# Performance work log

Hardware: AMD Instinct MI355X
Metric: run time of the kernel (lower is better)

Reference implementation:

```python
import jax, jax.numpy as jnp
import numpy as np

N = 100000   # nodes
E = 600000   # edges
K = 3        # TAGConv hops
EPS = 1e-5   # BatchNorm eps
SLOPE = 0.01 # LeakyReLU negative slope


def setup_inputs() -> dict:
    key = jax.random.key(0)
    ks = jax.random.split(key, 8)
    y = jax.random.normal(ks[0], (N, 128), dtype=jnp.float32)
    edge_index = jax.random.randint(ks[1], (2, E), 0, N, dtype=jnp.int64)
    edge_attr = jax.random.uniform(ks[2], (E,), dtype=jnp.float32)
    # TAGConv layer l has (K+1) weight matrices [in, out]; bias only on first two layers
    W1 = 0.1 * jax.random.normal(ks[3], (K + 1, 128, 128), dtype=jnp.float32)
    b1 = jnp.full((128,), 0.1, dtype=jnp.float32)
    W2 = 0.1 * jax.random.normal(ks[4], (K + 1, 128, 128), dtype=jnp.float32)
    b2 = jnp.full((128,), 0.1, dtype=jnp.float32)
    W3 = 0.1 * jax.random.normal(ks[5], (K + 1, 128, 64), dtype=jnp.float32)
    g1 = jnp.ones((128,), jnp.float32); be1 = jnp.zeros((128,), jnp.float32)
    g2 = jnp.ones((128,), jnp.float32); be2 = jnp.zeros((128,), jnp.float32)
    g3 = jnp.ones((64,), jnp.float32);  be3 = jnp.zeros((64,), jnp.float32)
    return dict(y=y, edge_index=edge_index, edge_attr=edge_attr,
                W1=W1, b1=b1, g1=g1, be1=be1,
                W2=W2, b2=b2, g2=g2, be2=be2,
                W3=W3, g3=g3, be3=be3)


def _tag_conv(x, W, b, src, dst, norm):
    # out = sum_{k=0..K} A_hat^k x @ W_k (+ b)
    out = x @ W[0]
    h = x
    for k in range(1, W.shape[0]):
        h = jax.ops.segment_sum(norm[:, None] * h[src], dst, num_segments=N)
        out = out + h @ W[k]
    return out if b is None else out + b


def _bn(x, g, b):
    # BatchNorm1d training mode: biased batch stats over nodes
    m = x.mean(axis=0)
    v = jnp.mean((x - m) ** 2, axis=0)
    return (x - m) * jax.lax.rsqrt(v + EPS) * g + b


def reference(y, edge_index, edge_attr, W1, b1, g1, be1, W2, b2, g2, be2, W3, g3, be3):
    src, dst = edge_index[0], edge_index[1]
    # gcn_norm (symmetric, no self-loops): D^{-1/2} A D^{-1/2}
    deg = jax.ops.segment_sum(edge_attr, dst, num_segments=N)
    dis = jnp.where(deg > 0, jax.lax.rsqrt(jnp.maximum(deg, 1e-12)), 0.0)
    norm = dis[src] * edge_attr * dis[dst]
    lrelu = lambda t: jax.nn.leaky_relu(t, SLOPE)
    x = lrelu(_bn(_tag_conv(y, W1, b1, src, dst, norm), g1, be1))
    x = lrelu(_bn(_tag_conv(x, W2, b2, src, dst, norm), g2, be2))
    x = lrelu(_bn(_tag_conv(x, W3, None, src, dst, norm), g3, be3))
    return x
```

## Files before the change

### kernel.cpp

```cpp
#include <hip/hip_runtime.h>
#include <hip/hip_bf16.h>

typedef unsigned short b16;
typedef __attribute__((ext_vector_type(8))) unsigned short us8;
typedef __attribute__((ext_vector_type(8))) short short8;
typedef __attribute__((ext_vector_type(4))) float float4v;

#define NN 100000
#define NE 600000

__device__ __forceinline__ float bf2f(b16 u) {
    return __uint_as_float(((unsigned)u) << 16);
}
__device__ __forceinline__ b16 f2bf(float f) {
    unsigned x = __float_as_uint(f);
    return (b16)((x + 0x7fffu + ((x >> 16) & 1u)) >> 16);
}

__global__ void k_detect(const void* __restrict__ y, const void* __restrict__ ei,
                         int* __restrict__ flags) {
    if (threadIdx.x == 0 && blockIdx.x == 0) {
        const b16* p = (const b16*)y;
        int f32 = 0;
        for (int i = 0; i < 128; ++i) {
            float v = bf2f(p[i]);
            if (!(fabsf(v) < 1e4f)) { f32 = 1; break; }
        }
        flags[0] = f32;
        const long long* q = (const long long*)ei;
        int i64 = 1;
        for (int i = 0; i < 4; ++i) {
            long long v = q[i];
            if (v < 0 || v >= NN) i64 = 0;
        }
        flags[1] = i64;
    }
}

__global__ void k_cvt(const void* __restrict__ in, float* __restrict__ out, int n,
                      const int* __restrict__ flags) {
    int i = blockIdx.x * blockDim.x + threadIdx.x;
    if (i >= n) return;
    out[i] = flags[0] ? ((const float*)in)[i] : bf2f(((const b16*)in)[i]);
}

__global__ void k_idx(const void* __restrict__ ei, int* __restrict__ src32,
                      int* __restrict__ dst32, const int* __restrict__ flags) {
    int e = blockIdx.x * blockDim.x + threadIdx.x;
    if (e >= NE) return;
    int s, d;
    if (flags[1]) {
        const long long* p = (const long long*)ei;
        s = (int)p[e];
        d = (int)p[NE + e];
    } else {
        const int* p = (const int*)ei;
        s = p[e];
        d = p[NE + e];
    }
    src32[e] = ((unsigned)s < NN) ? s : 0;
    dst32[e] = ((unsigned)d < NN) ? d : 0;
}

__global__ void k_degcnt(const int* __restrict__ dst, const void* __restrict__ ea,
                         float* __restrict__ deg, int* __restrict__ cnt,
                         const int* __restrict__ flags) {
    int e = blockIdx.x * blockDim.x + threadIdx.x;
    if (e >= NE) return;
    float w = flags[0] ? ((const float*)ea)[e] : bf2f(((const b16*)ea)[e]);
    int d = dst[e];
    unsafeAtomicAdd(&deg[d], w);
    atomicAdd(&cnt[d], 1);
}

__global__ void k_dis(float* deg) {
    int n = blockIdx.x * blockDim.x + threadIdx.x;
    if (n < NN) {
        float d = deg[n];
        deg[n] = (d > 0.f) ? rsqrtf(fmaxf(d, 1e-12f)) : 0.f;
    }
}

#define SCAN_B 1024
#define SCAN_NB ((NN + SCAN_B - 1) / SCAN_B)

__global__ __launch_bounds__(SCAN_B) void k_scan1(const int* __restrict__ cnt,
                                                  int* __restrict__ inc,
                                                  int* __restrict__ bsum) {
    __shared__ int s[SCAN_B];
    int i = blockIdx.x * SCAN_B + threadIdx.x;
    s[threadIdx.x] = (i < NN) ? cnt[i] : 0;
    __syncthreads();
    for (int off = 1; off < SCAN_B; off <<= 1) {
        int t = (threadIdx.x >= off) ? s[threadIdx.x - off] : 0;
        __syncthreads();
        s[threadIdx.x] += t;
        __syncthreads();
    }
    if (i < NN) inc[i] = s[threadIdx.x];
    if (threadIdx.x == SCAN_B - 1) bsum[blockIdx.x] = s[SCAN_B - 1];
}

__global__ void k_scan2(int* bsum) {
    if (threadIdx.x == 0 && blockIdx.x == 0) {
        int a = 0;
        for (int i = 0; i < SCAN_NB; ++i) {
            int t = bsum[i];
            bsum[i] = a;
            a += t;
        }
    }
}

__global__ void k_scan3(const int* __restrict__ inc, const int* __restrict__ bsum,
                        int* __restrict__ rowptr) {
    int i = blockIdx.x * blockDim.x + threadIdx.x;
    if (i == 0) rowptr[0] = 0;
    if (i < NN) rowptr[i + 1] = inc[i] + bsum[i / SCAN_B];
}

__global__ void k_fill(const int* __restrict__ src, const int* __restrict__ dst,
                       const void* __restrict__ ea, const float* __restrict__ dis,
                       const int* __restrict__ rowptr, int* __restrict__ fill,
                       int* __restrict__ csrc, float* __restrict__ cw,
                       const int* __restrict__ flags) {
    int e = blockIdx.x * blockDim.x + threadIdx.x;
    if (e >= NE) return;
    float a = flags[0] ? ((const float*)ea)[e] : bf2f(((const b16*)ea)[e]);
    int d = dst[e];
    int s = src[e];
    int pos = rowptr[d] + atomicAdd(&fill[d], 1);
    csrc[pos] = s;
    cw[pos] = dis[s] * a * dis[d];
}

__global__ void k_pack(const void* __restrict__ W, b16* __restrict__ Wp, int NC,
                       const int* __restrict__ flags) {
    int f = blockIdx.x * blockDim.x + threadIdx.x;
    int total = 512 * NC / 8;
    if (f >= total) return;
    int lane = f & 63;
    int rest = f >> 6;
    int CT = NC >> 4;
    int ct = rest % CT, ks = rest / CT;
    int k0 = 32 * ks + (lane >> 4) * 8;
    int col = 16 * ct + (lane & 15);
    us8 v;
#pragma unroll
    for (int j = 0; j < 8; ++j) {
        float x = flags[0] ? ((const float*)W)[(size_t)(k0 + j) * NC + col]
                           : bf2f(((const b16*)W)[(size_t)(k0 + j) * NC + col]);
        v[j] = f2bf(x);
    }
    *(us8*)&Wp[(size_t)f * 8] = v;
}

__global__ void k_cast(const void* __restrict__ y, b16* __restrict__ XC,
                       const int* __restrict__ flags) {
    int i = blockIdx.x * blockDim.x + threadIdx.x;
    if (i >= NN * 32) return;
    int row = i >> 5, cg = i & 31;
    float4 v;
    if (flags[0]) {
        v = ((const float4*)y)[i];
    } else {
        ushort4 u = ((const ushort4*)y)[i];
        v = make_float4(bf2f(u.x), bf2f(u.y), bf2f(u.z), bf2f(u.w));
    }
    ushort4 o;
    o.x = f2bf(v.x); o.y = f2bf(v.y); o.z = f2bf(v.z); o.w = f2bf(v.w);
    *(ushort4*)&XC[(size_t)row * 512 + 4 * cg] = o;
}

__global__ __launch_bounds__(256) void k_spmm(b16* __restrict__ XC, int ci, int co,
                                              const int* __restrict__ rowptr,
                                              const int* __restrict__ csrc,
                                              const float* __restrict__ cw) {
    int gid = blockIdx.x * blockDim.x + threadIdx.x;
    int node = gid >> 6;
    if (node >= NN) return;
    int lane = gid & 63;
    int grp = lane >> 4;
    int l15 = lane & 15;
    int beg = rowptr[node], end = rowptr[node + 1];

    float a0[8], a1[8];
#pragma unroll
    for (int j = 0; j < 8; ++j) {
        a0[j] = 0.f;
        a1[j] = 0.f;
    }
    int i = beg;
    for (; i + 7 < end; i += 8) {
        int e0 = i + grp, e1 = i + 4 + grp;
        int s0 = csrc[e0];
        float w0 = cw[e0];
        int s1 = csrc[e1];
        float w1 = cw[e1];
        us8 u0 = *(const us8*)&XC[(size_t)s0 * 512 + ci + 8 * l15];
        us8 u1 = *(const us8*)&XC[(size_t)s1 * 512 + ci + 8 * l15];
#pragma unroll
        for (int j = 0; j < 8; ++j) {
            a0[j] = fmaf(w0, bf2f(u0[j]), a0[j]);
            a1[j] = fmaf(w1, bf2f(u1[j]), a1[j]);
        }
    }
    for (; i < end; i += 4) {
        int e = i + grp;
        bool act = e < end;
        int ee = act ? e : (end - 1);
        float w = act ? cw[ee] : 0.f;
        int s = csrc[ee];
        us8 u = *(const us8*)&XC[(size_t)s * 512 + ci + 8 * l15];
#pragma unroll
        for (int j = 0; j < 8; ++j) a0[j] = fmaf(w, bf2f(u[j]), a0[j]);
    }
#pragma unroll
    for (int j = 0; j < 8; ++j) a0[j] += a1[j];
#pragma unroll
    for (int j = 0; j < 8; ++j) a0[j] += __shfl_xor(a0[j], 16);
#pragma unroll
    for (int j = 0; j < 8; ++j) a0[j] += __shfl_xor(a0[j], 32);
    if (grp == 0) {
        us8 o;
#pragma unroll
        for (int j = 0; j < 8; ++j) o[j] = f2bf(a0[j]);
        *(us8*)&XC[(size_t)node * 512 + co + 8 * l15] = o;
    }
}

template <int NC>
__global__ __launch_bounds__(256) void k_mgemm(const b16* __restrict__ XC,
                                               const b16* __restrict__ Wp,
                                               const float* __restrict__ bias,
                                               b16* __restrict__ OUT,
                                               float* __restrict__ gsum,
                                               float* __restrict__ gsq) {
    constexpr int CT = NC / 16;
    __shared__ b16 As[2][64 * 40];
    __shared__ b16 Bs[2][CT * 512];
    __shared__ float csum[NC], csq[NC];
    const int tid = threadIdx.x;
    const int wave = tid >> 6;
    const int lane = tid & 63;
    const int row0 = blockIdx.x * 64;
    const int quad = lane >> 4;
    const int l15 = lane & 15;

    float4v acc[CT];
#pragma unroll
    for (int ct = 0; ct < CT; ++ct) acc[ct] = (float4v)(0.f);
    for (int i = tid; i < NC; i += 256) {
        csum[i] = 0.f;
        csq[i] = 0.f;
    }

    const int arow = tid >> 2;
    const int apart = tid & 3;
    int grow = row0 + arow;
    if (grow >= NN) grow = NN - 1;
    const b16* gA = XC + (size_t)grow * 512 + apart * 8;
    b16* lA0 = &As[0][arow * 40 + apart * 8];
    b16* lA1 = &As[1][arow * 40 + apart * 8];

    *(us8*)lA0 = *(const us8*)gA;
    {
        const us8* gB = (const us8*)Wp;
#pragma unroll
        for (int q = 0; q < CT * 64 / 256; ++q)
            ((us8*)Bs[0])[q * 256 + tid] = gB[q * 256 + tid];
    }

    for (int ks = 0; ks < 16; ++ks) {
        int buf = ks & 1;
        __syncthreads();
        if (ks < 15) {
            *(us8*)(buf ? lA0 : lA1) = *(const us8*)(gA + 32 * (ks + 1));
            const us8* gB = (const us8*)(Wp + (size_t)(ks + 1) * CT * 512);
#pragma unroll
            for (int q = 0; q < CT * 64 / 256; ++q)
                ((us8*)Bs[buf ^ 1])[q * 256 + tid] = gB[q * 256 + tid];
        }
        short8 af = *(const short8*)&As[buf][(wave * 16 + l15) * 40 + quad * 8];
#pragma unroll
        for (int ct = 0; ct < CT; ++ct) {
            short8 bf = *(const short8*)&Bs[buf][ct * 512 + lane * 8];
            acc[ct] = __builtin_amdgcn_mfma_f32_16x16x32_bf16(af, bf, acc[ct], 0, 0, 0);
        }
    }

#pragma unroll
    for (int ct = 0; ct < CT; ++ct) {
        int col = 16 * ct + l15;
        float bv = bias ? bias[col] : 0.f;
        float s = 0.f, sq = 0.f;
#pragma unroll
        for (int r = 0; r < 4; ++r) {
            int row = row0 + wave * 16 + quad * 4 + r;
            if (row < NN) {
                float v = acc[ct][r] + bv;
                OUT[(size_t)row * NC + col] = f2bf(v);
                s += v;
                sq += v * v;
            }
        }
        s += __shfl_xor(s, 16);
        s += __shfl_xor(s, 32);
        sq += __shfl_xor(sq, 16);
        sq += __shfl_xor(sq, 32);
        if (quad == 0) {
            atomicAdd(&csum[col], s);
            atomicAdd(&csq[col], sq);
        }
    }
    __syncthreads();
    for (int i = tid; i < NC; i += 256) {
        unsafeAtomicAdd(&gsum[i], csum[i]);
        unsafeAtomicAdd(&gsq[i], csq[i]);
    }
}

__global__ void k_bnparam(const float* gsum, const float* gsq, const float* g,
                          const float* be, float* scale, float* shift, int ncols) {
    int c = threadIdx.x;
    if (c < ncols) {
        float m = gsum[c] * (1.f / NN);
        float v = gsq[c] * (1.f / NN) - m * m;
        v = fmaxf(v, 0.f);
        float s = rsqrtf(v + 1e-5f) * g[c];
        scale[c] = s;
        shift[c] = be[c] - m * s;
    }
}

__global__ void k_bnapply_mid(const b16* __restrict__ OUT,
                              const float* __restrict__ scale,
                              const float* __restrict__ shift, b16* __restrict__ XC) {
    int i = blockIdx.x * blockDim.x + threadIdx.x;
    if (i >= NN * 64) return;
    int row = i >> 6, c = (i & 63) * 2;
    ushort2 u = *(const ushort2*)&OUT[(size_t)row * 128 + c];
    float a = fmaf(bf2f(u.x), scale[c], shift[c]);
    float b = fmaf(bf2f(u.y), scale[c + 1], shift[c + 1]);
    a = a > 0.f ? a : 0.01f * a;
    b = b > 0.f ? b : 0.01f * b;
    ushort2 o;
    o.x = f2bf(a);
    o.y = f2bf(b);
    *(ushort2*)&XC[(size_t)row * 512 + c] = o;
}

__global__ void k_bnapply_last(const b16* __restrict__ OUT,
                               const float* __restrict__ scale,
                               const float* __restrict__ shift, void* __restrict__ dout,
                               const int* __restrict__ flags) {
    int i = blockIdx.x * blockDim.x + threadIdx.x;
    if (i >= NN * 64) return;
    int c = i & 63;
    float v = fmaf(bf2f(OUT[i]), scale[c], shift[c]);
    v = v > 0.f ? v : 0.01f * v;
    if (flags[0])
        ((float*)dout)[i] = v;
    else
        ((b16*)dout)[i] = f2bf(v);
}

#define PB_B1 0
#define PB_B2 128
#define PB_G1 256
#define PB_BE1 384
#define PB_G2 512
#define PB_BE2 640
#define PB_G3 768
#define PB_BE3 832
#define PB_SZ 896

extern "C" void kernel_launch(void* const* d_in, const int* in_sizes, int n_in,
                              void* d_out, int out_size, void* d_ws, size_t ws_size,
                              hipStream_t stream) {
    const void* y   = d_in[0];
    const void* ei  = d_in[1];
    const void* ea  = d_in[2];
    const void* W1  = d_in[3];
    const void* b1  = d_in[4];
    const void* g1  = d_in[5];
    const void* be1 = d_in[6];
    const void* W2  = d_in[7];
    const void* b2  = d_in[8];
    const void* g2  = d_in[9];
    const void* be2 = d_in[10];
    const void* W3  = d_in[11];
    const void* g3  = d_in[12];
    const void* be3 = d_in[13];

    char* w = (char*)d_ws;
    size_t used = 0;
    auto carve = [&](size_t bytes) -> char* {
        char* p = w + used;
        used += (bytes + 255) & ~(size_t)255;
        return p;
    };

    int* flags   = (int*)carve(16);
    int* src32   = (int*)carve((size_t)NE * 4);
    int* dst32   = (int*)carve((size_t)NE * 4);
    float* deg   = (float*)carve((size_t)NN * 4);
    int* cnt     = (int*)carve((size_t)NN * 4);
    int* rowptr  = (int*)carve((size_t)(NN + 1) * 4);
    int* cscan   = (int*)carve((size_t)NN * 4);
    int* bsum    = (int*)carve((size_t)SCAN_NB * 4);
    int* csrc    = (int*)carve((size_t)NE * 4);
    float* cw    = (float*)carve((size_t)NE * 4);
    float* PB    = (float*)carve(PB_SZ * 4);
    b16* Wp1     = (b16*)carve((size_t)512 * 128 * 2);
    b16* Wp2     = (b16*)carve((size_t)512 * 128 * 2);
    b16* Wp3     = (b16*)carve((size_t)512 * 64 * 2);
    b16* OUT     = (b16*)carve((size_t)NN * 128 * 2);
    float* gsum  = (float*)carve(128 * 4);
    float* gsq   = (float*)carve(128 * 4);
    float* scale = (float*)carve(128 * 4);
    float* shift = (float*)carve(128 * 4);
    b16* XC      = (b16*)carve((size_t)NN * 512 * 2);

    k_detect<<<1, 64, 0, stream>>>(y, ei, flags);
    auto cvt = [&](const void* in, float* out, int n) {
        k_cvt<<<(n + 127) / 128, 128, 0, stream>>>(in, out, n, flags);
    };
    cvt(b1, PB + PB_B1, 128);
    cvt(b2, PB + PB_B2, 128);
    cvt(g1, PB + PB_G1, 128);
    cvt(be1, PB + PB_BE1, 128);
    cvt(g2, PB + PB_G2, 128);
    cvt(be2, PB + PB_BE2, 128);
    cvt(g3, PB + PB_G3, 64);
    cvt(be3, PB + PB_BE3, 64);
    k_pack<<<(512 * 128 / 8 + 255) / 256, 256, 0, stream>>>(W1, Wp1, 128, flags);
    k_pack<<<(512 * 128 / 8 + 255) / 256, 256, 0, stream>>>(W2, Wp2, 128, flags);
    k_pack<<<(512 * 64 / 8 + 255) / 256, 256, 0, stream>>>(W3, Wp3, 64, flags);

    k_idx<<<(NE + 255) / 256, 256, 0, stream>>>(ei, src32, dst32, flags);
    hipMemsetAsync(deg, 0, (size_t)NN * 4, stream);
    hipMemsetAsync(cnt, 0, (size_t)NN * 4, stream);
    k_degcnt<<<(NE + 255) / 256, 256, 0, stream>>>(dst32, ea, deg, cnt, flags);
    k_dis<<<(NN + 255) / 256, 256, 0, stream>>>(deg);
    k_scan1<<<SCAN_NB, SCAN_B, 0, stream>>>(cnt, cscan, bsum);
    k_scan2<<<1, 64, 0, stream>>>(bsum);
    k_scan3<<<(NN + 255) / 256, 256, 0, stream>>>(cscan, bsum, rowptr);
    hipMemsetAsync(cnt, 0, (size_t)NN * 4, stream);
    k_fill<<<(NE + 255) / 256, 256, 0, stream>>>(src32, dst32, ea, deg, rowptr, cnt,
                                                 csrc, cw, flags);

    k_cast<<<(NN * 32 + 255) / 256, 256, 0, stream>>>(y, XC, flags);

    auto spmm = [&](int ci, int co) {
        k_spmm<<<(NN * 64 + 255) / 256, 256, 0, stream>>>(XC, ci, co, rowptr, csrc, cw);
    };
    const int gemm_grid = (NN + 63) / 64;

    auto layer = [&](const b16* Wp, const float* bias, const float* g, const float* be,
                     int NC, bool last) {
        spmm(0, 128);
        spmm(128, 256);
        spmm(256, 384);
        hipMemsetAsync(gsum, 0, NC * 4, stream);
        hipMemsetAsync(gsq, 0, NC * 4, stream);
        if (NC == 128)
            k_mgemm<128><<<gemm_grid, 256, 0, stream>>>(XC, Wp, bias, OUT, gsum, gsq);
        else
            k_mgemm<64><<<gemm_grid, 256, 0, stream>>>(XC, Wp, bias, OUT, gsum, gsq);
        k_bnparam<<<1, NC, 0, stream>>>(gsum, gsq, g, be, scale, shift, NC);
        if (last)
            k_bnapply_last<<<(NN * 64 + 255) / 256, 256, 0, stream>>>(OUT, scale, shift,
                                                                      d_out, flags);
        else
            k_bnapply_mid<<<(NN * 64 + 255) / 256, 256, 0, stream>>>(OUT, scale, shift,
                                                                     XC);
    };

    layer(Wp1, PB + PB_B1, PB + PB_G1, PB + PB_BE1, 128, false);
    layer(Wp2, PB + PB_B2, PB + PB_G2, PB + PB_BE2, 128, false);
    layer(Wp3, nullptr, PB + PB_G3, PB + PB_BE3, 64, true);
}
```

Before: 800.8 us.

## Load GEMM fragments straight to registers and unroll SpMM by four edges

The fused multi-hop GEMM no longer stages A and B tiles in LDS. Each wave now loads its MFMA fragments directly from global memory into registers with a one-step software prefetch, and handles two 16-row tiles so B fragments are reused, which halves the grid. The SpMM inner loop now processes 16 edges per iteration with predicated loads and drops the separate tail loop, to raise memory-level parallelism. The trade-offs are redundant global B loads per wave with no LDS sharing, higher register pressure, and wasted loads on nodes with few edges.

```diff
diff --git a/kernel.cpp b/kernel.cpp
--- a/kernel.cpp
+++ b/kernel.cpp
@@ -190,30 +190,28 @@
         a0[j] = 0.f;
         a1[j] = 0.f;
     }
-    int i = beg;
-    for (; i + 7 < end; i += 8) {
-        int e0 = i + grp, e1 = i + 4 + grp;
-        int s0 = csrc[e0];
-        float w0 = cw[e0];
-        int s1 = csrc[e1];
-        float w1 = cw[e1];
+    for (int i = beg; i < end; i += 16) {
+        int e0 = i + grp, e1 = i + 4 + grp, e2 = i + 8 + grp, e3 = i + 12 + grp;
+        float w0 = (e0 < end) ? cw[e0] : 0.f;
+        float w1 = (e1 < end) ? cw[e1] : 0.f;
+        float w2 = (e2 < end) ? cw[e2] : 0.f;
+        float w3 = (e3 < end) ? cw[e3] : 0.f;
+        int lim = end - 1;
+        int s0 = csrc[e0 < lim ? e0 : lim];
+        int s1 = csrc[e1 < lim ? e1 : lim];
+        int s2 = csrc[e2 < lim ? e2 : lim];
+        int s3 = csrc[e3 < lim ? e3 : lim];
         us8 u0 = *(const us8*)&XC[(size_t)s0 * 512 + ci + 8 * l15];
         us8 u1 = *(const us8*)&XC[(size_t)s1 * 512 + ci + 8 * l15];
+        us8 u2 = *(const us8*)&XC[(size_t)s2 * 512 + ci + 8 * l15];
+        us8 u3 = *(const us8*)&XC[(size_t)s3 * 512 + ci + 8 * l15];
 #pragma unroll
         for (int j = 0; j < 8; ++j) {
             a0[j] = fmaf(w0, bf2f(u0[j]), a0[j]);
             a1[j] = fmaf(w1, bf2f(u1[j]), a1[j]);
-        }
-    }
-    for (; i < end; i += 4) {
-        int e = i + grp;
-        bool act = e < end;
-        int ee = act ? e : (end - 1);
-        float w = act ? cw[ee] : 0.f;
-        int s = csrc[ee];
-        us8 u = *(const us8*)&XC[(size_t)s * 512 + ci + 8 * l15];
-#pragma unroll
-        for (int j = 0; j < 8; ++j) a0[j] = fmaf(w, bf2f(u[j]), a0[j]);
+            a0[j] = fmaf(w2, bf2f(u2[j]), a0[j]);
+            a1[j] = fmaf(w3, bf2f(u3[j]), a1[j]);
+        }
     }
 #pragma unroll
     for (int j = 0; j < 8; ++j) a0[j] += a1[j];
@@ -237,80 +235,88 @@
                                                float* __restrict__ gsum,
                                                float* __restrict__ gsq) {
     constexpr int CT = NC / 16;
-    __shared__ b16 As[2][64 * 40];
-    __shared__ b16 Bs[2][CT * 512];
     __shared__ float csum[NC], csq[NC];
     const int tid = threadIdx.x;
     const int wave = tid >> 6;
     const int lane = tid & 63;
-    const int row0 = blockIdx.x * 64;
     const int quad = lane >> 4;
     const int l15 = lane & 15;
-
-    float4v acc[CT];
-#pragma unroll
-    for (int ct = 0; ct < CT; ++ct) acc[ct] = (float4v)(0.f);
+    const int rbase = blockIdx.x * 128 + wave * 32;
+
     for (int i = tid; i < NC; i += 256) {
         csum[i] = 0.f;
         csq[i] = 0.f;
     }
 
-    const int arow = tid >> 2;
-    const int apart = tid & 3;
-    int grow = row0 + arow;
-    if (grow >= NN) grow = NN - 1;
-    const b16* gA = XC + (size_t)grow * 512 + apart * 8;
-    b16* lA0 = &As[0][arow * 40 + apart * 8];
-    b16* lA1 = &As[1][arow * 40 + apart * 8];
-
-    *(us8*)lA0 = *(const us8*)gA;
-    {
-        const us8* gB = (const us8*)Wp;
-#pragma unroll
-        for (int q = 0; q < CT * 64 / 256; ++q)
-            ((us8*)Bs[0])[q * 256 + tid] = gB[q * 256 + tid];
-    }
+    float4v acc[2][CT];
+#pragma unroll
+    for (int rt = 0; rt < 2; ++rt)
+#pragma unroll
+        for (int ct = 0; ct < CT; ++ct) acc[rt][ct] = (float4v)(0.f);
+
+    const b16* gA[2];
+#pragma unroll
+    for (int rt = 0; rt < 2; ++rt) {
+        int r = rbase + 16 * rt + l15;
+        if (r >= NN) r = NN - 1;
+        gA[rt] = XC + (size_t)r * 512 + quad * 8;
+    }
+    const b16* gB = Wp + lane * 8;
+
+    short8 afc[2], bfc[CT], afn[2], bfn[CT];
+#pragma unroll
+    for (int rt = 0; rt < 2; ++rt) afc[rt] = *(const short8*)(gA[rt]);
+#pragma unroll
+    for (int ct = 0; ct < CT; ++ct) bfc[ct] = *(const short8*)(gB + ct * 512);
 
     for (int ks = 0; ks < 16; ++ks) {
-        int buf = ks & 1;
-        __syncthreads();
         if (ks < 15) {
-            *(us8*)(buf ? lA0 : lA1) = *(const us8*)(gA + 32 * (ks + 1));
-            const us8* gB = (const us8*)(Wp + (size_t)(ks + 1) * CT * 512);
-#pragma unroll
-            for (int q = 0; q < CT * 64 / 256; ++q)
-                ((us8*)Bs[buf ^ 1])[q * 256 + tid] = gB[q * 256 + tid];
-        }
-        short8 af = *(const short8*)&As[buf][(wave * 16 + l15) * 40 + quad * 8];
+#pragma unroll
+            for (int rt = 0; rt < 2; ++rt)
+                afn[rt] = *(const short8*)(gA[rt] + 32 * (ks + 1));
+#pragma unroll
+            for (int ct = 0; ct < CT; ++ct)
+                bfn[ct] = *(const short8*)(gB + (size_t)((ks + 1) * CT + ct) * 512);
+        }
+#pragma unroll
+        for (int rt = 0; rt < 2; ++rt)
+#pragma unroll
+            for (int ct = 0; ct < CT; ++ct)
+                acc[rt][ct] = __builtin_amdgcn_mfma_f32_16x16x32_bf16(
+                    afc[rt], bfc[ct], acc[rt][ct], 0, 0, 0);
+        if (ks < 15) {
+#pragma unroll
+            for (int rt = 0; rt < 2; ++rt) afc[rt] = afn[rt];
+#pragma unroll
+            for (int ct = 0; ct < CT; ++ct) bfc[ct] = bfn[ct];
+        }
+    }
+
+#pragma unroll
+    for (int rt = 0; rt < 2; ++rt) {
 #pragma unroll
         for (int ct = 0; ct < CT; ++ct) {
-            short8 bf = *(const short8*)&Bs[buf][ct * 512 + lane * 8];
-            acc[ct] = __builtin_amdgcn_mfma_f32_16x16x32_bf16(af, bf, acc[ct], 0, 0, 0);
-        }
-    }
-
-#pragma unroll
-    for (int ct = 0; ct < CT; ++ct) {
-        int col = 16 * ct + l15;
-        float bv = bias ? bias[col] : 0.f;
-        float s = 0.f, sq = 0.f;
-#pragma unroll
-        for (int r = 0; r < 4; ++r) {
-            int row = row0 + wave * 16 + quad * 4 + r;
-            if (row < NN) {
-                float v = acc[ct][r] + bv;
-                OUT[(size_t)row * NC + col] = f2bf(v);
-                s += v;
-                sq += v * v;
+            int col = 16 * ct + l15;
+            float bv = bias ? bias[col] : 0.f;
+            float s = 0.f, sq = 0.f;
+#pragma unroll
+            for (int r = 0; r < 4; ++r) {
+                int row = rbase + 16 * rt + quad * 4 + r;
+                if (row < NN) {
+                    float v = acc[rt][ct][r] + bv;
+                    OUT[(size_t)row * NC + col] = f2bf(v);
+                    s += v;
+                    sq += v * v;
+                }
             }
-        }
-        s += __shfl_xor(s, 16);
-        s += __shfl_xor(s, 32);
-        sq += __shfl_xor(sq, 16);
-        sq += __shfl_xor(sq, 32);
-        if (quad == 0) {
-            atomicAdd(&csum[col], s);
-            atomicAdd(&csq[col], sq);
+            s += __shfl_xor(s, 16);
+            s += __shfl_xor(s, 32);
+            sq += __shfl_xor(sq, 16);
+            sq += __shfl_xor(sq, 32);
+            if (quad == 0) {
+                atomicAdd(&csum[col], s);
+                atomicAdd(&csq[col], sq);
+            }
         }
     }
     __syncthreads();
@@ -455,7 +461,7 @@
     auto spmm = [&](int ci, int co) {
         k_spmm<<<(NN * 64 + 255) / 256, 256, 0, stream>>>(XC, ci, co, rowptr, csrc, cw);
     };
-    const int gemm_grid = (NN + 63) / 64;
+    const int gemm_grid = (NN + 127) / 128;
 
     auto layer = [&](const b16* Wp, const float* bias, const float* g, const float* be,
                      int NC, bool last) {
```

Measured after the change: 791.4 us. Within noise of the previous version (-1.2%).
